# Kernel tuning notes

Measured on AMD Instinct MI355X. Metric: run time of the kernel, lower is better.

Reference implementation:

```python
import jax, jax.numpy as jnp
import numpy as np

DIM = 1280
HEADS = 16
HEAD_DIM = DIM // HEADS  # 80
N_CHUNKS = 8
CHUNK = 1024
TOTAL = N_CHUNKS * CHUNK  # 8192 packed tokens


def rotate_half(x):
    x1, x2 = jnp.split(x, 2, axis=-1)
    return jnp.concatenate([-x2, x1], axis=-1)


def setup_inputs() -> dict:
    key = jax.random.key(0)
    k0, k1, k2 = jax.random.split(key, 3)
    hidden_states = jax.random.normal(k0, (TOTAL, DIM), dtype=jnp.float32)
    # 2D-rope style per-token angles, duplicated halves (standard vision RoPE layout)
    inv_freq = 1.0 / (10000.0 ** (jnp.arange(0, HEAD_DIM, 2, dtype=jnp.float32) / HEAD_DIM))
    pos = jnp.arange(TOTAL, dtype=jnp.float32)
    freqs = pos[:, None] * inv_freq[None, :]            # [T, HEAD_DIM//2]
    emb = jnp.concatenate([freqs, freqs], axis=-1)      # [T, HEAD_DIM]
    cos = jnp.cos(emb)
    sin = jnp.sin(emb)
    qkv_w = jax.random.normal(k1, (3 * DIM, DIM), dtype=jnp.float32) * 0.02
    qkv_b = jnp.zeros((3 * DIM,), dtype=jnp.float32)
    proj_w = jax.random.normal(k2, (DIM, DIM), dtype=jnp.float32) * 0.02
    proj_b = jnp.zeros((DIM,), dtype=jnp.float32)
    cu_seqlens = (jnp.arange(N_CHUNKS + 1, dtype=jnp.int32) * CHUNK)
    return {"hidden_states": hidden_states, "cos": cos, "sin": sin,
            "qkv_w": qkv_w, "qkv_b": qkv_b, "proj_w": proj_w, "proj_b": proj_b,
            "cu_seqlens": cu_seqlens}


def reference(hidden_states, cos, sin, qkv_w, qkv_b, proj_w, proj_b, cu_seqlens):
    # Equal-length chunks (cu_seqlens uniform): vectorize the Python chunk loop
    # as a leading batch axis n over chunks of length L.
    n = cu_seqlens.shape[0] - 1
    total, dim = hidden_states.shape
    L = total // n
    scaling = HEAD_DIM ** -0.5

    x = hidden_states.reshape(n, L, dim)
    qkv = x @ qkv_w.T + qkv_b                              # [n, L, 3*dim]
    qkv = qkv.reshape(n, L, 3, HEADS, HEAD_DIM)
    q, k, v = qkv[:, :, 0], qkv[:, :, 1], qkv[:, :, 2]     # [n, L, H, hd]

    # inline RoPE in fp32 (matches apply_rotary_pos_emb_vision)
    c = cos.reshape(n, L, 1, HEAD_DIM).astype(jnp.float32)
    s = sin.reshape(n, L, 1, HEAD_DIM).astype(jnp.float32)
    qf = q.astype(jnp.float32)
    kf = k.astype(jnp.float32)
    q = (qf * c + rotate_half(qf) * s).astype(q.dtype)
    k = (kf * c + rotate_half(kf) * s).astype(k.dtype)

    # naive per-chunk full attention: QK^T, fp32 softmax, PV
    scores = jnp.einsum('nlhd,nmhd->nhlm', q, k) * scaling  # [n, H, L, L]
    probs = jax.nn.softmax(scores.astype(jnp.float32), axis=-1).astype(q.dtype)
    out = jnp.einsum('nhlm,nmhd->nlhd', probs, v)           # [n, L, H, hd]
    out = out.reshape(n, L, dim)
    out = out @ proj_w.T + proj_b                           # [n, L, dim]
    return out.reshape(total, dim)
```

## Files before the change

### kernel.cpp

```cpp
#include <hip/hip_runtime.h>
#include <stdint.h>

#define DIM 1280
#define HEADS 16
#define HD 80
#define TOTAL 8192
#define CHUNK 1024
#define QKVN 3840

typedef __attribute__((ext_vector_type(8))) __bf16 bf16x8;
typedef __attribute__((ext_vector_type(4))) float floatx4;

typedef __attribute__((address_space(1))) const uint32_t gu32;
typedef __attribute__((address_space(3))) uint32_t lu32;

__device__ __forceinline__ void llds16(const void* g, void* l) {
  __builtin_amdgcn_global_load_lds((gu32*)g, (lu32*)l, 16, 0, 0);
}

__device__ __forceinline__ unsigned short f2b(float f) {
  union { __bf16 b; unsigned short u; } x; x.b = (__bf16)f; return x.u;
}
__device__ __forceinline__ float b2f(unsigned short u) {
  union { __bf16 b; unsigned short u; } x; x.u = u; return (float)x.b;
}
__device__ __forceinline__ float fexp2(float x) {
#if __has_builtin(__builtin_amdgcn_exp2f)
  return __builtin_amdgcn_exp2f(x);
#else
  return __expf(x * 0.6931471805599453f);
#endif
}

#define QSCALE (0.11180339887498949f * 1.44269504088896340f)

#define QROW 96
#define KT_SH (64 * 104)
#define VT_SH (80 * 72)

__global__ void cvt_bf16(const float* __restrict__ src, unsigned short* __restrict__ dst, int n4) {
  int i = blockIdx.x * 256 + threadIdx.x;
  if (i >= n4) return;
  float4 v = reinterpret_cast<const float4*>(src)[i];
  ushort4 o;
  o.x = f2b(v.x); o.y = f2b(v.y); o.z = f2b(v.z); o.w = f2b(v.w);
  reinterpret_cast<ushort4*>(dst)[i] = o;
}


__device__ __forceinline__ void stage_a64(const unsigned short* __restrict__ G,
                                          unsigned short* ls, int wv, int lane,
                                          int row0, int kk, int hi) {
#pragma unroll
  for (int t = 0; t < 2; ++t) {
    const int stripe = t * 8 + wv;
    const int rb = ((stripe >> 3) << 7) + ((stripe & 7) << 3) + hi;
    const int r = rb + (lane >> 3);
    const int ch = (lane & 7) ^ (r & 7);
    llds16(G + (size_t)(row0 + r) * DIM + kk + (ch << 3), ls + rb * 64);
  }
}

__device__ __forceinline__ void stage_b64(const unsigned short* __restrict__ G,
                                          unsigned short* ls, int wv, int lane,
                                          int row0, int kk, int hi) {
#pragma unroll
  for (int t = 0; t < 2; ++t) {
    const int stripe = t * 8 + wv;
    const int rb = ((stripe >> 2) << 6) + ((stripe & 3) << 3) + hi;
    const int r = rb + (lane >> 3);
    const int ch = (lane & 7) ^ (r & 7);
    llds16(G + (size_t)(row0 + r) * DIM + kk + (ch << 3), ls + rb * 64);
  }
}

__device__ __forceinline__ bf16x8 frg(const unsigned short* ls, int r, int cx) {
  return *reinterpret_cast<const bf16x8*>(ls + r * 64 + (cx << 3));
}

#define MFMA_BF16 __builtin_amdgcn_mfma_f32_16x16x32_bf16

template<int MODE>
__launch_bounds__(512, 2)
__global__ void gemm8(const unsigned short* __restrict__ A,
                      const unsigned short* __restrict__ B,
                      const float* __restrict__ bias,
                      unsigned short* __restrict__ qo,
                      unsigned short* __restrict__ ko,
                      unsigned short* __restrict__ vo,
                      float* __restrict__ fo) {
  __shared__ __attribute__((aligned(16))) unsigned short lsA[2][256 * 64];
  __shared__ __attribute__((aligned(16))) unsigned short lsB[2][256 * 64];
  const int m0 = blockIdx.x * 256;
  const int n0 = blockIdx.y * 256;
  const int tid = threadIdx.x;
  const int wv = tid >> 6, lane = tid & 63;
  const int wr = wv >> 2, wc = wv & 3;
  const int q4 = lane >> 4, l15 = lane & 15;
  const int sx = l15 & 7;
  const int cx0 = q4 ^ sx;
  const int cx1 = (4 + q4) ^ sx;

  stage_a64(A, &lsA[0][0], wv, lane, m0, 0, 0);
  stage_b64(B, &lsB[0][0], wv, lane, n0, 0, 0);
  stage_b64(B, &lsB[0][0], wv, lane, n0, 0, 32);
  stage_a64(A, &lsA[0][0], wv, lane, m0, 0, 64);
  stage_b64(B, &lsB[1][0], wv, lane, n0, 64, 0);
  stage_a64(A, &lsA[1][0], wv, lane, m0, 64, 0);
  stage_b64(B, &lsB[1][0], wv, lane, n0, 64, 32);

  floatx4 acc[8][4];
#pragma unroll
  for (int i = 0; i < 8; ++i)
#pragma unroll
    for (int j = 0; j < 4; ++j)
      acc[i][j] = (floatx4){0.f, 0.f, 0.f, 0.f};

  asm volatile("s_waitcnt vmcnt(6)" ::: "memory");
  __builtin_amdgcn_s_barrier();

  const int rA = wr * 128 + l15;
  const int rB = wc * 64 + l15;

#pragma unroll 2
  for (int kt = 0; kt < 20; ++kt) {
    const unsigned short* la = &lsA[kt & 1][0];
    const unsigned short* lb = &lsB[kt & 1][0];
    unsigned short* aN = &lsA[(kt & 1) ^ 1][0];
    unsigned short* aC = &lsA[kt & 1][0];
    unsigned short* bC = &lsB[kt & 1][0];
    const bool st1 = (kt + 1 < 20);
    const bool st2 = (kt + 2 < 20);

    bf16x8 Ar[4][2], Blo[2][2], Bhi[2][2];

#pragma unroll
    for (int m = 0; m < 4; ++m) {
      Ar[m][0] = frg(la, rA + m * 16, cx0);
      Ar[m][1] = frg(la, rA + m * 16, cx1);
    }
#pragma unroll
    for (int n = 0; n < 2; ++n) {
      Blo[n][0] = frg(lb, rB + n * 16, cx0);
      Blo[n][1] = frg(lb, rB + n * 16, cx1);
    }
    if (st1) stage_a64(A, aN, wv, lane, m0, (kt + 1) * 64, 64);
    asm volatile("s_waitcnt lgkmcnt(8)" ::: "memory");
    __builtin_amdgcn_s_barrier();
    asm volatile("s_waitcnt lgkmcnt(0)" ::: "memory");
    __builtin_amdgcn_sched_barrier(0);
    __builtin_amdgcn_s_setprio(1);
#pragma unroll
    for (int m = 0; m < 4; ++m)
#pragma unroll
      for (int n = 0; n < 2; ++n) {
        acc[m][n] = MFMA_BF16(Ar[m][0], Blo[n][0], acc[m][n], 0, 0, 0);
        acc[m][n] = MFMA_BF16(Ar[m][1], Blo[n][1], acc[m][n], 0, 0, 0);
      }
    __builtin_amdgcn_s_setprio(0);
    __builtin_amdgcn_s_barrier();

#pragma unroll
    for (int n = 0; n < 2; ++n) {
      Bhi[n][0] = frg(lb, rB + (n + 2) * 16, cx0);
      Bhi[n][1] = frg(lb, rB + (n + 2) * 16, cx1);
    }
    if (st2) stage_b64(B, bC, wv, lane, n0, (kt + 2) * 64, 0);
    __builtin_amdgcn_s_barrier();
    asm volatile("s_waitcnt lgkmcnt(0)" ::: "memory");
    __builtin_amdgcn_sched_barrier(0);
    __builtin_amdgcn_s_setprio(1);
#pragma unroll
    for (int m = 0; m < 4; ++m)
#pragma unroll
      for (int n = 0; n < 2; ++n) {
        acc[m][n + 2] = MFMA_BF16(Ar[m][0], Bhi[n][0], acc[m][n + 2], 0, 0, 0);
        acc[m][n + 2] = MFMA_BF16(Ar[m][1], Bhi[n][1], acc[m][n + 2], 0, 0, 0);
      }
    __builtin_amdgcn_s_setprio(0);
    __builtin_amdgcn_s_barrier();

#pragma unroll
    for (int m = 0; m < 4; ++m) {
      Ar[m][0] = frg(la, rA + (m + 4) * 16, cx0);
      Ar[m][1] = frg(la, rA + (m + 4) * 16, cx1);
    }
    if (st2) stage_a64(A, aC, wv, lane, m0, (kt + 2) * 64, 0);
    __builtin_amdgcn_s_barrier();
    asm volatile("s_waitcnt lgkmcnt(0)" ::: "memory");
    __builtin_amdgcn_sched_barrier(0);
    __builtin_amdgcn_s_setprio(1);
#pragma unroll
    for (int m = 0; m < 4; ++m)
#pragma unroll
      for (int n = 0; n < 2; ++n) {
        acc[m + 4][n + 2] = MFMA_BF16(Ar[m][0], Bhi[n][0], acc[m + 4][n + 2], 0, 0, 0);
        acc[m + 4][n + 2] = MFMA_BF16(Ar[m][1], Bhi[n][1], acc[m + 4][n + 2], 0, 0, 0);
      }
    __builtin_amdgcn_s_setprio(0);
    __builtin_amdgcn_s_barrier();

    if (st2) stage_b64(B, bC, wv, lane, n0, (kt + 2) * 64, 32);
    __builtin_amdgcn_s_setprio(1);
#pragma unroll
    for (int m = 0; m < 4; ++m)
#pragma unroll
      for (int n = 0; n < 2; ++n) {
        acc[m + 4][n] = MFMA_BF16(Ar[m][0], Blo[n][0], acc[m + 4][n], 0, 0, 0);
        acc[m + 4][n] = MFMA_BF16(Ar[m][1], Blo[n][1], acc[m + 4][n], 0, 0, 0);
      }
    __builtin_amdgcn_s_setprio(0);

    if (st2)      asm volatile("s_waitcnt vmcnt(6)" ::: "memory");
    else if (st1) asm volatile("s_waitcnt vmcnt(0)" ::: "memory");
    if (st1) __builtin_amdgcn_s_barrier();
  }

  unsigned short* os = nullptr;
  int nloc = n0;
  if (MODE == 0) {
    if (blockIdx.y < 5)       { os = qo; }
    else if (blockIdx.y < 10) { os = ko; nloc = n0 - DIM; }
    else                      { os = vo; nloc = n0 - 2 * DIM; }
  }
#pragma unroll
  for (int n = 0; n < 4; ++n) {
    const int cg = wc * 64 + n * 16 + l15;
    const float bn = bias[n0 + cg];
#pragma unroll
    for (int m = 0; m < 8; ++m) {
#pragma unroll
      for (int r = 0; r < 4; ++r) {
        const int row = m0 + wr * 128 + m * 16 + q4 * 4 + r;
        const float val = acc[m][n][r] + bn;
        if (MODE == 0) os[(size_t)row * DIM + nloc + cg] = f2b(val);
        else           fo[(size_t)row * DIM + n0 + cg] = val;
      }
    }
  }
}

__global__ void prep_q(const unsigned short* __restrict__ qbuf,
                       const float* __restrict__ cp, const float* __restrict__ sp,
                       unsigned short* __restrict__ qimg) {
  const int m = blockIdx.x, tid = threadIdx.x;
  const int ch = m >> 10, rl = m & 1023;
#pragma unroll
  for (int i = 0; i < 3; ++i) {
    const int it = i * 256 + tid;
    if (it < 640) {
      const int h = it / 40, d = it - h * 40;
      const float c = cp[m * HD + d], s = sp[m * HD + d];
      const float x1 = b2f(qbuf[(size_t)m * DIM + h * HD + d]);
      const float x2 = b2f(qbuf[(size_t)m * DIM + h * HD + d + 40]);
      const size_t ob = ((size_t)(ch * 16 + h) * 1024 + rl) * QROW;
      qimg[ob + d]      = f2b((x1 * c - x2 * s) * QSCALE);
      qimg[ob + d + 40] = f2b((x2 * c + x1 * s) * QSCALE);
    }
  }
  { const int h = tid >> 4, c = tid & 15;
    qimg[((size_t)(ch * 16 + h) * 1024 + rl) * QROW + 80 + c] = 0; }
}

__global__ void prep_k(const unsigned short* __restrict__ kbuf,
                       const float* __restrict__ cp, const float* __restrict__ sp,
                       unsigned short* __restrict__ kimg) {
  const int m = blockIdx.x, tid = threadIdx.x;
  const int ch = m >> 10, rl = m & 1023;
  const int jt = rl >> 6, rr = rl & 63;
#pragma unroll
  for (int i = 0; i < 3; ++i) {
    const int it = i * 256 + tid;
    if (it < 640) {
      const int h = it / 40, d = it - h * 40;
      const float c = cp[m * HD + d], s = sp[m * HD + d];
      const float x1 = b2f(kbuf[(size_t)m * DIM + h * HD + d]);
      const float x2 = b2f(kbuf[(size_t)m * DIM + h * HD + d + 40]);
      const size_t ob = ((size_t)((ch * 16 + h) * 16 + jt) * KT_SH) + rr * 104;
      kimg[ob + d]      = f2b(x1 * c - x2 * s);
      kimg[ob + d + 40] = f2b(x2 * c + x1 * s);
    }
  }
#pragma unroll
  for (int i = 0; i < 2; ++i) {
    const int it = i * 256 + tid;
    if (it < 384) {
      const int h = it / 24, c = it - h * 24;
      kimg[((size_t)((ch * 16 + h) * 16 + jt) * KT_SH) + rr * 104 + 80 + c] = 0;
    }
  }
}

__global__ void prep_v(const unsigned short* __restrict__ vbuf,
                       unsigned short* __restrict__ vimg) {
  __shared__ __attribute__((aligned(16))) unsigned short lsT[64 * 88];
  const int bx = blockIdx.x;
  const int jt = bx & 15, h = (bx >> 4) & 15, ch = bx >> 8;
  const int tid = threadIdx.x;
  const int row0 = ch * CHUNK + jt * 64;
#pragma unroll
  for (int i = 0; i < 3; ++i) {
    const int it = i * 256 + tid;
    if (it < 640) {
      const int r = it / 10, c = it - r * 10;
      const uint4 v = *reinterpret_cast<const uint4*>(vbuf + (size_t)(row0 + r) * DIM + h * HD + c * 8);
      *reinterpret_cast<uint4*>(&lsT[r * 88 + c * 8]) = v;
    }
  }
  __syncthreads();
  unsigned short* ot = vimg + (size_t)((ch * 16 + h) * 16 + jt) * VT_SH;
#pragma unroll
  for (int i = 0; i < 12; ++i) {
    const int it = i * 256 + tid;
    if (it < 2880) {
      const int d = it / 36, kk = it - d * 36;
      uint32_t w = 0;
      if (kk < 32) {
        const uint32_t lo = lsT[(2 * kk) * 88 + d];
        const uint32_t hi = lsT[(2 * kk + 1) * 88 + d];
        w = lo | (hi << 16);
      }
      *reinterpret_cast<uint32_t*>(ot + d * 72 + kk * 2) = w;
    }
  }
}

__launch_bounds__(256, 3)
__global__ void attn_k(const unsigned short* __restrict__ qimg,
                       const unsigned short* __restrict__ kimg,
                       const unsigned short* __restrict__ vimg,
                       unsigned short* __restrict__ ob) {
  __shared__ __attribute__((aligned(16))) unsigned short lsK[KT_SH];
  __shared__ __attribute__((aligned(16))) unsigned short lsV[VT_SH];
  __shared__ __attribute__((aligned(16))) unsigned short lsP[128 * 72];

  const int bx = blockIdx.x;
  const int qt = bx & 7, h = (bx >> 3) & 15, ch = bx >> 7;
  const int tid = threadIdx.x, wv = tid >> 6, lane = tid & 63;
  const int q4 = lane >> 4, l15 = lane & 15;
  const int qrow_loc = qt * 128 + wv * 32;

  bf16x8 aq[2][3];
  {
    const unsigned short* qb = qimg + ((size_t)(ch * 16 + h) * 1024 + qrow_loc) * QROW;
#pragma unroll
    for (int mt = 0; mt < 2; ++mt)
#pragma unroll
      for (int ks = 0; ks < 3; ++ks)
        aq[mt][ks] = *reinterpret_cast<const bf16x8*>(qb + (size_t)(mt * 16 + l15) * QROW + ks * 32 + q4 * 8);
  }

  floatx4 oacc[2][5];
  float lpart[2] = {0.f, 0.f};
#pragma unroll
  for (int mt = 0; mt < 2; ++mt)
#pragma unroll
    for (int t = 0; t < 5; ++t) oacc[mt][t] = (floatx4){0.f, 0.f, 0.f, 0.f};

  const char* kbase = (const char*)(kimg + (size_t)(ch * 16 + h) * 16 * KT_SH);
  const char* vbase = (const char*)(vimg + (size_t)(ch * 16 + h) * 16 * VT_SH);

  for (int jt = 0; jt < 16; ++jt) {
    __syncthreads();
    {
      const char* kg = kbase + (size_t)jt * (KT_SH * 2);
#pragma unroll
      for (int r = 0; r < 4; ++r) {
        const int off = (r * 4 + wv) * 1024;
        if (off < KT_SH * 2)
          llds16(kg + off + lane * 16, (char*)lsK + off);
      }
      const char* vg = vbase + (size_t)jt * (VT_SH * 2);
#pragma unroll
      for (int r = 0; r < 3; ++r) {
        const int off = (r * 4 + wv) * 1024;
        if (off < VT_SH * 2) {
          if (off + 1024 <= VT_SH * 2) llds16(vg + off + lane * 16, (char*)lsV + off);
          else if (lane < 16)          llds16(vg + off + lane * 16, (char*)lsV + off);
        }
      }
    }
    __syncthreads();

    floatx4 sfr[2][4];
#pragma unroll
    for (int c = 0; c < 4; ++c) {
      const bf16x8 ak0 = *reinterpret_cast<const bf16x8*>(&lsK[(c * 16 + l15) * 104 + 0  + q4 * 8]);
      const bf16x8 ak1 = *reinterpret_cast<const bf16x8*>(&lsK[(c * 16 + l15) * 104 + 32 + q4 * 8]);
      const bf16x8 ak2 = *reinterpret_cast<const bf16x8*>(&lsK[(c * 16 + l15) * 104 + 64 + q4 * 8]);
#pragma unroll
      for (int mt = 0; mt < 2; ++mt) {
        floatx4 s = (floatx4){0.f, 0.f, 0.f, 0.f};
        s = __builtin_amdgcn_mfma_f32_16x16x32_bf16(ak0, aq[mt][0], s, 0, 0, 0);
        s = __builtin_amdgcn_mfma_f32_16x16x32_bf16(ak1, aq[mt][1], s, 0, 0, 0);
        s = __builtin_amdgcn_mfma_f32_16x16x32_bf16(ak2, aq[mt][2], s, 0, 0, 0);
        sfr[mt][c] = s;
      }
    }

#pragma unroll
    for (int mt = 0; mt < 2; ++mt)
#pragma unroll
      for (int c = 0; c < 4; ++c) {
        const float p0 = fexp2(sfr[mt][c][0]);
        const float p1 = fexp2(sfr[mt][c][1]);
        const float p2 = fexp2(sfr[mt][c][2]);
        const float p3 = fexp2(sfr[mt][c][3]);
        lpart[mt] += (p0 + p1) + (p2 + p3);
        ushort4 w;
        w.x = f2b(p0); w.y = f2b(p1); w.z = f2b(p2); w.w = f2b(p3);
        *reinterpret_cast<ushort4*>(&lsP[(wv * 32 + mt * 16 + l15) * 72 + c * 16 + q4 * 4]) = w;
      }

#pragma unroll
    for (int ks = 0; ks < 2; ++ks) {
      const bf16x8 ap0 = *reinterpret_cast<const bf16x8*>(&lsP[(wv * 32 + 0  + l15) * 72 + ks * 32 + q4 * 8]);
      const bf16x8 ap1 = *reinterpret_cast<const bf16x8*>(&lsP[(wv * 32 + 16 + l15) * 72 + ks * 32 + q4 * 8]);
#pragma unroll
      for (int t = 0; t < 5; ++t) {
        const bf16x8 bv = *reinterpret_cast<const bf16x8*>(&lsV[(t * 16 + l15) * 72 + ks * 32 + q4 * 8]);
        oacc[0][t] = __builtin_amdgcn_mfma_f32_16x16x32_bf16(ap0, bv, oacc[0][t], 0, 0, 0);
        oacc[1][t] = __builtin_amdgcn_mfma_f32_16x16x32_bf16(ap1, bv, oacc[1][t], 0, 0, 0);
      }
    }
  }

#pragma unroll
  for (int mt = 0; mt < 2; ++mt) {
    lpart[mt] += __shfl_xor(lpart[mt], 16, 64);
    lpart[mt] += __shfl_xor(lpart[mt], 32, 64);
  }
  float inv[2];
  inv[0] = 1.0f / lpart[0];
  inv[1] = 1.0f / lpart[1];

  float invr[2][4];
#pragma unroll
  for (int mt = 0; mt < 2; ++mt)
#pragma unroll
    for (int r = 0; r < 4; ++r)
      invr[mt][r] = __shfl(inv[mt], q4 * 4 + r, 64);

#pragma unroll
  for (int mt = 0; mt < 2; ++mt)
#pragma unroll
    for (int t = 0; t < 5; ++t)
#pragma unroll
      for (int r = 0; r < 4; ++r) {
        const int gr = ch * CHUNK + qrow_loc + mt * 16 + q4 * 4 + r;
        const int gc = h * HD + t * 16 + l15;
        ob[(size_t)gr * DIM + gc] = f2b(oacc[mt][t][r] * invr[mt][r]);
      }
}

extern "C" void kernel_launch(void* const* d_in, const int* in_sizes, int n_in,
                              void* d_out, int out_size, void* d_ws, size_t ws_size,
                              hipStream_t stream) {
  (void)in_sizes; (void)n_in; (void)out_size; (void)ws_size;
  const float* hs    = (const float*)d_in[0];
  const float* cosp  = (const float*)d_in[1];
  const float* sinp  = (const float*)d_in[2];
  const float* qkvw  = (const float*)d_in[3];
  const float* qkvb  = (const float*)d_in[4];
  const float* projw = (const float*)d_in[5];
  const float* projb = (const float*)d_in[6];

  char* ws = (char*)d_ws;
  unsigned short* xb   = (unsigned short*)(ws + 0);
  unsigned short* wq   = (unsigned short*)(ws + 20971520);
  unsigned short* qbuf = (unsigned short*)(ws + 30801920);
  unsigned short* kbuf = (unsigned short*)(ws + 51773440);
  unsigned short* vbuf = (unsigned short*)(ws + 72744960);
  unsigned short* wp   = (unsigned short*)(ws + 93716480);
  unsigned short* obuf = (unsigned short*)(ws + 96993280);
  unsigned short* kimg = (unsigned short*)(ws + 117964800);
  unsigned short* qimg = (unsigned short*)(ws + 0);
  unsigned short* vimg = (unsigned short*)(ws + 30801920);

  cvt_bf16<<<TOTAL * DIM / 4 / 256, 256, 0, stream>>>(hs, xb, TOTAL * DIM / 4);
  cvt_bf16<<<QKVN * DIM / 4 / 256, 256, 0, stream>>>(qkvw, wq, QKVN * DIM / 4);
  cvt_bf16<<<DIM * DIM / 4 / 256, 256, 0, stream>>>(projw, wp, DIM * DIM / 4);

  gemm8<0><<<dim3(TOTAL / 256, QKVN / 256), 512, 0, stream>>>(
      xb, wq, qkvb, qbuf, kbuf, vbuf, nullptr);

  prep_q<<<TOTAL, 256, 0, stream>>>(qbuf, cosp, sinp, qimg);
  prep_k<<<TOTAL, 256, 0, stream>>>(kbuf, cosp, sinp, kimg);
  prep_v<<<2048, 256, 0, stream>>>(vbuf, vimg);

  attn_k<<<1024, 256, 0, stream>>>(qimg, kimg, vimg, obuf);

  gemm8<1><<<dim3(TOTAL / 256, DIM / 256), 512, 0, stream>>>(
      obuf, wp, projb, nullptr, nullptr, nullptr, (float*)d_out);
}
```

Baseline: 362.0 us.

## Software-pipeline last MFMA quadrant into next k-iteration and cut barriers

Moves the fourth MFMA quadrant (ArHi x Blo) of each k-step to the start of the next iteration, with an epilogue after the loop. Its MFMAs can then overlap the next tile's LDS fragment reads and global stages. The change also removes most s_setprio and sched_barrier calls plus several extra barriers, keeping one wait-then-barrier per phase. Holding the A and B fragments across iterations raises register pressure, and dropping the priority and scheduling hints may let the compiler interleave work less favourably.

```diff
diff --git a/kernel.cpp b/kernel.cpp
--- a/kernel.cpp
+++ b/kernel.cpp
@@ -79,6 +79,8 @@
 }
 
 #define MFMA_BF16 __builtin_amdgcn_mfma_f32_16x16x32_bf16
+#define LGKM0() asm volatile("s_waitcnt lgkmcnt(0)" ::: "memory")
+#define BARR()  asm volatile("s_barrier" ::: "memory")
 
 template<int MODE>
 __launch_bounds__(512, 2)
@@ -117,10 +119,12 @@
       acc[i][j] = (floatx4){0.f, 0.f, 0.f, 0.f};
 
   asm volatile("s_waitcnt vmcnt(6)" ::: "memory");
-  __builtin_amdgcn_s_barrier();
+  BARR();
 
   const int rA = wr * 128 + l15;
   const int rB = wc * 64 + l15;
+
+  bf16x8 ArLo[4][2], ArHi[4][2], Blo[2][2], Bhi[2][2];
 
 #pragma unroll 2
   for (int kt = 0; kt < 20; ++kt) {
@@ -132,12 +136,19 @@
     const bool st1 = (kt + 1 < 20);
     const bool st2 = (kt + 2 < 20);
 
-    bf16x8 Ar[4][2], Blo[2][2], Bhi[2][2];
-
+    if (kt > 0) {
+#pragma unroll
+      for (int m = 0; m < 4; ++m)
+#pragma unroll
+        for (int n = 0; n < 2; ++n) {
+          acc[m + 4][n] = MFMA_BF16(ArHi[m][0], Blo[n][0], acc[m + 4][n], 0, 0, 0);
+          acc[m + 4][n] = MFMA_BF16(ArHi[m][1], Blo[n][1], acc[m + 4][n], 0, 0, 0);
+        }
+    }
 #pragma unroll
     for (int m = 0; m < 4; ++m) {
-      Ar[m][0] = frg(la, rA + m * 16, cx0);
-      Ar[m][1] = frg(la, rA + m * 16, cx1);
+      ArLo[m][0] = frg(la, rA + m * 16, cx0);
+      ArLo[m][1] = frg(la, rA + m * 16, cx1);
     }
 #pragma unroll
     for (int n = 0; n < 2; ++n) {
@@ -145,76 +156,61 @@
       Blo[n][1] = frg(lb, rB + n * 16, cx1);
     }
     if (st1) stage_a64(A, aN, wv, lane, m0, (kt + 1) * 64, 64);
-    asm volatile("s_waitcnt lgkmcnt(8)" ::: "memory");
-    __builtin_amdgcn_s_barrier();
-    asm volatile("s_waitcnt lgkmcnt(0)" ::: "memory");
-    __builtin_amdgcn_sched_barrier(0);
-    __builtin_amdgcn_s_setprio(1);
+    LGKM0();
+    BARR();
+
 #pragma unroll
     for (int m = 0; m < 4; ++m)
 #pragma unroll
       for (int n = 0; n < 2; ++n) {
-        acc[m][n] = MFMA_BF16(Ar[m][0], Blo[n][0], acc[m][n], 0, 0, 0);
-        acc[m][n] = MFMA_BF16(Ar[m][1], Blo[n][1], acc[m][n], 0, 0, 0);
-      }
-    __builtin_amdgcn_s_setprio(0);
-    __builtin_amdgcn_s_barrier();
-
+        acc[m][n] = MFMA_BF16(ArLo[m][0], Blo[n][0], acc[m][n], 0, 0, 0);
+        acc[m][n] = MFMA_BF16(ArLo[m][1], Blo[n][1], acc[m][n], 0, 0, 0);
+      }
 #pragma unroll
     for (int n = 0; n < 2; ++n) {
       Bhi[n][0] = frg(lb, rB + (n + 2) * 16, cx0);
       Bhi[n][1] = frg(lb, rB + (n + 2) * 16, cx1);
     }
     if (st2) stage_b64(B, bC, wv, lane, n0, (kt + 2) * 64, 0);
-    __builtin_amdgcn_s_barrier();
-    asm volatile("s_waitcnt lgkmcnt(0)" ::: "memory");
-    __builtin_amdgcn_sched_barrier(0);
-    __builtin_amdgcn_s_setprio(1);
+    LGKM0();
+    BARR();
+
 #pragma unroll
     for (int m = 0; m < 4; ++m)
 #pragma unroll
       for (int n = 0; n < 2; ++n) {
-        acc[m][n + 2] = MFMA_BF16(Ar[m][0], Bhi[n][0], acc[m][n + 2], 0, 0, 0);
-        acc[m][n + 2] = MFMA_BF16(Ar[m][1], Bhi[n][1], acc[m][n + 2], 0, 0, 0);
-      }
-    __builtin_amdgcn_s_setprio(0);
-    __builtin_amdgcn_s_barrier();
-
+        acc[m][n + 2] = MFMA_BF16(ArLo[m][0], Bhi[n][0], acc[m][n + 2], 0, 0, 0);
+        acc[m][n + 2] = MFMA_BF16(ArLo[m][1], Bhi[n][1], acc[m][n + 2], 0, 0, 0);
+      }
 #pragma unroll
     for (int m = 0; m < 4; ++m) {
-      Ar[m][0] = frg(la, rA + (m + 4) * 16, cx0);
-      Ar[m][1] = frg(la, rA + (m + 4) * 16, cx1);
+      ArHi[m][0] = frg(la, rA + (m + 4) * 16, cx0);
+      ArHi[m][1] = frg(la, rA + (m + 4) * 16, cx1);
     }
     if (st2) stage_a64(A, aC, wv, lane, m0, (kt + 2) * 64, 0);
-    __builtin_amdgcn_s_barrier();
-    asm volatile("s_waitcnt lgkmcnt(0)" ::: "memory");
-    __builtin_amdgcn_sched_barrier(0);
-    __builtin_amdgcn_s_setprio(1);
+    LGKM0();
+    BARR();
+
 #pragma unroll
     for (int m = 0; m < 4; ++m)
 #pragma unroll
       for (int n = 0; n < 2; ++n) {
-        acc[m + 4][n + 2] = MFMA_BF16(Ar[m][0], Bhi[n][0], acc[m + 4][n + 2], 0, 0, 0);
-        acc[m + 4][n + 2] = MFMA_BF16(Ar[m][1], Bhi[n][1], acc[m + 4][n + 2], 0, 0, 0);
-      }
-    __builtin_amdgcn_s_setprio(0);
-    __builtin_amdgcn_s_barrier();
-
+        acc[m + 4][n + 2] = MFMA_BF16(ArHi[m][0], Bhi[n][0], acc[m + 4][n + 2], 0, 0, 0);
+        acc[m + 4][n + 2] = MFMA_BF16(ArHi[m][1], Bhi[n][1], acc[m + 4][n + 2], 0, 0, 0);
+      }
     if (st2) stage_b64(B, bC, wv, lane, n0, (kt + 2) * 64, 32);
-    __builtin_amdgcn_s_setprio(1);
-#pragma unroll
-    for (int m = 0; m < 4; ++m)
-#pragma unroll
-      for (int n = 0; n < 2; ++n) {
-        acc[m + 4][n] = MFMA_BF16(Ar[m][0], Blo[n][0], acc[m + 4][n], 0, 0, 0);
-        acc[m + 4][n] = MFMA_BF16(Ar[m][1], Blo[n][1], acc[m + 4][n], 0, 0, 0);
-      }
-    __builtin_amdgcn_s_setprio(0);
-
     if (st2)      asm volatile("s_waitcnt vmcnt(6)" ::: "memory");
     else if (st1) asm volatile("s_waitcnt vmcnt(0)" ::: "memory");
-    if (st1) __builtin_amdgcn_s_barrier();
-  }
+    BARR();
+  }
+
+#pragma unroll
+  for (int m = 0; m < 4; ++m)
+#pragma unroll
+    for (int n = 0; n < 2; ++n) {
+      acc[m + 4][n] = MFMA_BF16(ArHi[m][0], Blo[n][0], acc[m + 4][n], 0, 0, 0);
+      acc[m + 4][n] = MFMA_BF16(ArHi[m][1], Blo[n][1], acc[m + 4][n], 0, 0, 0);
+    }
 
   unsigned short* os = nullptr;
   int nloc = n0;
```

Result: faster. 351.4 us (-2.9%).
